# Kernel tuning notes

Measured on AMD Instinct MI355X. Metric: run time of the kernel, lower is better.

The kernel has to match this reference:

```python
import jax, jax.numpy as jnp
import numpy as np

B, H, S, DK = 2, 8, 4096, 64


def setup_inputs() -> dict:
    key = jax.random.key(0)
    kq, kk, kv = jax.random.split(key, 3)
    Q = jax.random.normal(kq, (B, H, S, DK), dtype=jnp.float32)
    K = jax.random.normal(kk, (B, H, S, DK), dtype=jnp.float32)
    V = jax.random.normal(kv, (B, H, S, DK), dtype=jnp.float32)
    attn_mask = jnp.zeros((1,), dtype=bool)  # accepted but unused by the module
    return {"Q": Q, "K": K, "V": V, "attn_mask": attn_mask}


def reference(Q, K, V, attn_mask):
    d_k = Q.shape[-1]
    scale = 1.0 / np.sqrt(d_k).astype(np.float32)
    # scores: [b, h, q, k] -- full O(n^2) matrix, as in the original
    scores = jnp.einsum('bhqd,bhkd->bhqk', Q, K) * scale
    attn = jax.nn.softmax(scores, axis=-1)
    context = jnp.einsum('bhqk,bhkd->bhqd', attn, V)
    return (context, attn)
```

## Files before the change

### kernel.cpp

```cpp
#include <hip/hip_runtime.h>
#include <hip/hip_bf16.h>


typedef __bf16 bf16x8 __attribute__((ext_vector_type(8)));
typedef __bf16 bf16x4 __attribute__((ext_vector_type(4)));
typedef float f32x4 __attribute__((ext_vector_type(4)));

#define BH 16
#define SEQ 4096
#define DKD 64
#define PSTRIDE 72
#define LOG2E 1.44269504088896f

__global__ void cvt_bf16_kernel(const float* __restrict__ src,
                                __bf16* __restrict__ dst, int n4, float scale) {
    int i = blockIdx.x * blockDim.x + threadIdx.x;
    if (i < n4) {
        const float4 v = reinterpret_cast<const float4*>(src)[i];
        bf16x4 o;
        o[0] = (__bf16)(v.x * scale); o[1] = (__bf16)(v.y * scale);
        o[2] = (__bf16)(v.z * scale); o[3] = (__bf16)(v.w * scale);
        reinterpret_cast<bf16x4*>(dst)[i] = o;
    }
}

__global__ void transpose_v_kernel(const float* __restrict__ V,
                                   __bf16* __restrict__ Vt) {
    __shared__ __bf16 T[DKD][72];
    const int head = blockIdx.y;
    const int s0 = blockIdx.x * 64;
    const int t = threadIdx.x;
    const float* vp = V + ((size_t)head * SEQ + s0) * DKD;
#pragma unroll
    for (int i = 0; i < 16; ++i) {
        int j = i * 256 + t;
        T[j & 63][j >> 6] = (__bf16)vp[j];
    }
    __syncthreads();
    __bf16* op = Vt + (size_t)head * DKD * SEQ + s0;
#pragma unroll
    for (int i = 0; i < 16; ++i) {
        int j = i * 256 + t;
        op[(size_t)(j >> 6) * SEQ + (j & 63)] = T[j >> 6][j & 63];
    }
}

__global__ __launch_bounds__(256, 4) void attn_kernel(
    const __bf16* __restrict__ Qb, const __bf16* __restrict__ Kb,
    const __bf16* __restrict__ Vt, float* __restrict__ out_ctx,
    float* __restrict__ out_attn) {
    __shared__ __align__(16) __bf16 Pl[2][4][16][PSTRIDE];

    const int tid = threadIdx.x;
    const int w = tid >> 6;
    const int lane = tid & 63;
    const int c16 = lane & 15;
    const int g = lane >> 4;

    const int wg = blockIdx.x;
    const int head = ((wg & 7) << 1) | ((wg >> 3) & 1);
    const int qt = wg >> 4;
    const int qbase = qt * 64 + w * 16;

    const __bf16* qp = Qb + ((size_t)head * SEQ + qbase + c16) * DKD + g * 8;
    const bf16x8 qf0 = *reinterpret_cast<const bf16x8*>(qp);
    const bf16x8 qf1 = *reinterpret_cast<const bf16x8*>(qp + 32);

    const __bf16* kbase = Kb + (size_t)head * SEQ * DKD;
    const __bf16* vbase = Vt + (size_t)head * DKD * SEQ;
    float* attn_p = out_attn + ((size_t)head * SEQ + qbase) * SEQ;

    float lsum = 0.f;
    auto loadK = [&](bf16x8 (&kf)[8], int tile) {
        const int kt = tile * 64;
#pragma unroll
        for (int ct = 0; ct < 4; ++ct) {
            const __bf16* kp = kbase + (size_t)(kt + ct * 16 + c16) * DKD + g * 8;
            kf[ct * 2] = *reinterpret_cast<const bf16x8*>(kp);
            kf[ct * 2 + 1] = *reinterpret_cast<const bf16x8*>(kp + 32);
        }
    };
    auto procA = [&](const bf16x8 (&kf)[8]) {
#pragma unroll
        for (int ct = 0; ct < 4; ++ct) {
            f32x4 a = (f32x4){0.f, 0.f, 0.f, 0.f};
            a = __builtin_amdgcn_mfma_f32_16x16x32_bf16(kf[ct * 2], qf0, a, 0, 0, 0);
            a = __builtin_amdgcn_mfma_f32_16x16x32_bf16(kf[ct * 2 + 1], qf1, a, 0, 0, 0);
            float e0 = __builtin_amdgcn_exp2f(a[0] * LOG2E);
            float e1 = __builtin_amdgcn_exp2f(a[1] * LOG2E);
            float e2 = __builtin_amdgcn_exp2f(a[2] * LOG2E);
            float e3 = __builtin_amdgcn_exp2f(a[3] * LOG2E);
            lsum += (e0 + e1) + (e2 + e3);
        }
    };
    {
        bf16x8 kA[8], kB[8];
        loadK(kA, 0);
        for (int t = 0; t < 64; t += 2) {
            loadK(kB, t + 1);
            procA(kA);
            loadK(kA, (t + 2) & 63);
            procA(kB);
        }
    }
    lsum += __shfl_xor(lsum, 16);
    lsum += __shfl_xor(lsum, 32);
    const float inv_l = __builtin_amdgcn_rcpf(lsum);

    f32x4 o[4];
#pragma unroll
    for (int dt = 0; dt < 4; ++dt) o[dt] = (f32x4){0.f, 0.f, 0.f, 0.f};

    auto computeS = [&](int tile, __bf16(*Pbuf)[PSTRIDE]) {
        const int kt = tile * 64;
        f32x4 acc[4];
#pragma unroll
        for (int ct = 0; ct < 4; ++ct) {
            acc[ct] = (f32x4){0.f, 0.f, 0.f, 0.f};
            const __bf16* kp = kbase + (size_t)(kt + ct * 16 + c16) * DKD + g * 8;
            bf16x8 kf0 = *reinterpret_cast<const bf16x8*>(kp);
            bf16x8 kf1 = *reinterpret_cast<const bf16x8*>(kp + 32);
            acc[ct] = __builtin_amdgcn_mfma_f32_16x16x32_bf16(kf0, qf0, acc[ct], 0, 0, 0);
            acc[ct] = __builtin_amdgcn_mfma_f32_16x16x32_bf16(kf1, qf1, acc[ct], 0, 0, 0);
        }
#pragma unroll
        for (int ct = 0; ct < 4; ++ct) {
            bf16x4 pb;
#pragma unroll
            for (int r = 0; r < 4; ++r)
                pb[r] = (__bf16)(__builtin_amdgcn_exp2f(acc[ct][r] * LOG2E) * inv_l);
            *reinterpret_cast<bf16x4*>(&Pbuf[c16][ct * 16 + g * 4]) = pb;
        }
    };

    auto storeAttn = [&](int tile, const __bf16(*Pbuf)[PSTRIDE]) {
        const int kt = tile * 64;
#pragma unroll
        for (int r4 = 0; r4 < 4; ++r4) {
            const int row = r4 * 4 + g;
            bf16x4 pb = *reinterpret_cast<const bf16x4*>(&Pbuf[row][c16 * 4]);
            f32x4 v;
#pragma unroll
            for (int j = 0; j < 4; ++j) v[j] = (float)pb[j];
            __builtin_nontemporal_store(
                v, reinterpret_cast<f32x4*>(attn_p + (size_t)row * SEQ + kt + c16 * 4));
        }
    };

    auto pvTile = [&](int tile, const __bf16(*Pbuf)[PSTRIDE]) {
        const int kt = tile * 64;
        bf16x8 pb0 = *reinterpret_cast<const bf16x8*>(&Pbuf[c16][g * 8]);
        bf16x8 pb1 = *reinterpret_cast<const bf16x8*>(&Pbuf[c16][g * 8 + 32]);
#pragma unroll
        for (int dt = 0; dt < 4; ++dt) {
            const __bf16* vp = vbase + (size_t)(dt * 16 + c16) * SEQ + kt + g * 8;
            bf16x8 vf0 = *reinterpret_cast<const bf16x8*>(vp);
            bf16x8 vf1 = *reinterpret_cast<const bf16x8*>(vp + 32);
            o[dt] = __builtin_amdgcn_mfma_f32_16x16x32_bf16(vf0, pb0, o[dt], 0, 0, 0);
            o[dt] = __builtin_amdgcn_mfma_f32_16x16x32_bf16(vf1, pb1, o[dt], 0, 0, 0);
        }
    };

    computeS(0, Pl[0][w]);
    for (int t = 1; t < 63; t += 2) {
        computeS(t, Pl[1][w]);
        storeAttn(t - 1, Pl[0][w]);
        pvTile(t - 1, Pl[0][w]);
        computeS(t + 1, Pl[0][w]);
        storeAttn(t, Pl[1][w]);
        pvTile(t, Pl[1][w]);
    }
    computeS(63, Pl[1][w]);
    storeAttn(62, Pl[0][w]);
    pvTile(62, Pl[0][w]);
    storeAttn(63, Pl[1][w]);
    pvTile(63, Pl[1][w]);

    float* ctx_p = out_ctx + ((size_t)head * SEQ + qbase) * DKD;
#pragma unroll
    for (int dt = 0; dt < 4; ++dt)
        *reinterpret_cast<f32x4*>(ctx_p + (size_t)c16 * DKD + dt * 16 + g * 4) = o[dt];
}

extern "C" void kernel_launch(void* const* d_in, const int* in_sizes, int n_in,
                              void* d_out, int out_size, void* d_ws, size_t ws_size,
                              hipStream_t stream) {
    const float* Q = (const float*)d_in[0];
    const float* K = (const float*)d_in[1];
    const float* V = (const float*)d_in[2];
    float* out = (float*)d_out;

    const size_t nElem = (size_t)BH * SEQ * DKD;
    __bf16* Qb = (__bf16*)d_ws;
    __bf16* Kb = Qb + nElem;
    __bf16* Vt = Kb + nElem;

    float* out_ctx = out;
    float* out_attn = out + nElem;

    const int n4 = (int)(nElem / 4);
    cvt_bf16_kernel<<<dim3((n4 + 255) / 256), dim3(256), 0, stream>>>(Q, Qb, n4, 0.125f);
    cvt_bf16_kernel<<<dim3((n4 + 255) / 256), dim3(256), 0, stream>>>(K, Kb, n4, 1.0f);
    transpose_v_kernel<<<dim3(64, BH), dim3(256), 0, stream>>>(V, Vt);
    attn_kernel<<<dim3(BH * SEQ / 64), dim3(256), 0, stream>>>(Qb, Kb, Vt, out_ctx, out_attn);
}
```

Measured before the change: 728.6 us.

## Split key range across wave pairs with cross-wave reduction of row sums and context

Each block now covers 32 query rows instead of 64. Two waves share each 16-row slice and each handles half of the key tiles. Row-sum partials are combined through shared memory after a barrier, and the partial context accumulators are reduced through LDS before the final write. The grid doubles and launch bounds are raised to 8 blocks per unit. The hand-pipelined K prefetch in the first pass is dropped, and attention stores become regular stores instead of nontemporal ones. Together these aim for more parallelism and occupancy, at the cost of extra barriers, LDS traffic and possible register pressure.

```diff
diff --git a/kernel.cpp b/kernel.cpp
--- a/kernel.cpp
+++ b/kernel.cpp
@@ -45,22 +45,26 @@
     }
 }
 
-__global__ __launch_bounds__(256, 4) void attn_kernel(
+__global__ __launch_bounds__(256, 8) void attn_kernel(
     const __bf16* __restrict__ Qb, const __bf16* __restrict__ Kb,
     const __bf16* __restrict__ Vt, float* __restrict__ out_ctx,
     float* __restrict__ out_attn) {
     __shared__ __align__(16) __bf16 Pl[2][4][16][PSTRIDE];
+    __shared__ float Lsum[4][16];
 
     const int tid = threadIdx.x;
     const int w = tid >> 6;
     const int lane = tid & 63;
     const int c16 = lane & 15;
     const int g = lane >> 4;
+    const int qsub = w & 1;
+    const int khalf = w >> 1;
 
     const int wg = blockIdx.x;
     const int head = ((wg & 7) << 1) | ((wg >> 3) & 1);
-    const int qt = wg >> 4;
-    const int qbase = qt * 64 + w * 16;
+    const int qblk = wg >> 4;
+    const int qbase = qblk * 32 + qsub * 16;
+    const int tile0 = khalf * 32;
 
     const __bf16* qp = Qb + ((size_t)head * SEQ + qbase + c16) * DKD + g * 8;
     const bf16x8 qf0 = *reinterpret_cast<const bf16x8*>(qp);
@@ -71,48 +75,35 @@
     float* attn_p = out_attn + ((size_t)head * SEQ + qbase) * SEQ;
 
     float lsum = 0.f;
-    auto loadK = [&](bf16x8 (&kf)[8], int tile) {
-        const int kt = tile * 64;
+    for (int t = 0; t < 32; ++t) {
+        const int kt = (tile0 + t) * 64;
 #pragma unroll
         for (int ct = 0; ct < 4; ++ct) {
             const __bf16* kp = kbase + (size_t)(kt + ct * 16 + c16) * DKD + g * 8;
-            kf[ct * 2] = *reinterpret_cast<const bf16x8*>(kp);
-            kf[ct * 2 + 1] = *reinterpret_cast<const bf16x8*>(kp + 32);
-        }
-    };
-    auto procA = [&](const bf16x8 (&kf)[8]) {
-#pragma unroll
-        for (int ct = 0; ct < 4; ++ct) {
+            bf16x8 kf0 = *reinterpret_cast<const bf16x8*>(kp);
+            bf16x8 kf1 = *reinterpret_cast<const bf16x8*>(kp + 32);
             f32x4 a = (f32x4){0.f, 0.f, 0.f, 0.f};
-            a = __builtin_amdgcn_mfma_f32_16x16x32_bf16(kf[ct * 2], qf0, a, 0, 0, 0);
-            a = __builtin_amdgcn_mfma_f32_16x16x32_bf16(kf[ct * 2 + 1], qf1, a, 0, 0, 0);
+            a = __builtin_amdgcn_mfma_f32_16x16x32_bf16(kf0, qf0, a, 0, 0, 0);
+            a = __builtin_amdgcn_mfma_f32_16x16x32_bf16(kf1, qf1, a, 0, 0, 0);
             float e0 = __builtin_amdgcn_exp2f(a[0] * LOG2E);
             float e1 = __builtin_amdgcn_exp2f(a[1] * LOG2E);
             float e2 = __builtin_amdgcn_exp2f(a[2] * LOG2E);
             float e3 = __builtin_amdgcn_exp2f(a[3] * LOG2E);
             lsum += (e0 + e1) + (e2 + e3);
         }
-    };
-    {
-        bf16x8 kA[8], kB[8];
-        loadK(kA, 0);
-        for (int t = 0; t < 64; t += 2) {
-            loadK(kB, t + 1);
-            procA(kA);
-            loadK(kA, (t + 2) & 63);
-            procA(kB);
-        }
     }
     lsum += __shfl_xor(lsum, 16);
     lsum += __shfl_xor(lsum, 32);
-    const float inv_l = __builtin_amdgcn_rcpf(lsum);
+    if (g == 0) Lsum[w][c16] = lsum;
+    __syncthreads();
+    const float inv_l = __builtin_amdgcn_rcpf(Lsum[w][c16] + Lsum[w ^ 2][c16]);
 
     f32x4 o[4];
 #pragma unroll
     for (int dt = 0; dt < 4; ++dt) o[dt] = (f32x4){0.f, 0.f, 0.f, 0.f};
 
-    auto computeS = [&](int tile, __bf16(*Pbuf)[PSTRIDE]) {
-        const int kt = tile * 64;
+    auto computeS = [&](int t, __bf16(*Pbuf)[PSTRIDE]) {
+        const int kt = (tile0 + t) * 64;
         f32x4 acc[4];
 #pragma unroll
         for (int ct = 0; ct < 4; ++ct) {
@@ -133,22 +124,8 @@
         }
     };
 
-    auto storeAttn = [&](int tile, const __bf16(*Pbuf)[PSTRIDE]) {
-        const int kt = tile * 64;
-#pragma unroll
-        for (int r4 = 0; r4 < 4; ++r4) {
-            const int row = r4 * 4 + g;
-            bf16x4 pb = *reinterpret_cast<const bf16x4*>(&Pbuf[row][c16 * 4]);
-            f32x4 v;
-#pragma unroll
-            for (int j = 0; j < 4; ++j) v[j] = (float)pb[j];
-            __builtin_nontemporal_store(
-                v, reinterpret_cast<f32x4*>(attn_p + (size_t)row * SEQ + kt + c16 * 4));
-        }
-    };
-
-    auto pvTile = [&](int tile, const __bf16(*Pbuf)[PSTRIDE]) {
-        const int kt = tile * 64;
+    auto pvTile = [&](int t, const __bf16(*Pbuf)[PSTRIDE]) {
+        const int kt = (tile0 + t) * 64;
         bf16x8 pb0 = *reinterpret_cast<const bf16x8*>(&Pbuf[c16][g * 8]);
         bf16x8 pb1 = *reinterpret_cast<const bf16x8*>(&Pbuf[c16][g * 8 + 32]);
 #pragma unroll
@@ -161,25 +138,52 @@
         }
     };
 
+    auto storeAttn = [&](int t, const __bf16(*Pbuf)[PSTRIDE]) {
+        const int kt = (tile0 + t) * 64;
+#pragma unroll
+        for (int r4 = 0; r4 < 4; ++r4) {
+            const int row = r4 * 4 + g;
+            bf16x4 pb = *reinterpret_cast<const bf16x4*>(&Pbuf[row][c16 * 4]);
+            f32x4 v;
+#pragma unroll
+            for (int j = 0; j < 4; ++j) v[j] = (float)pb[j];
+            *reinterpret_cast<f32x4*>(attn_p + (size_t)row * SEQ + kt + c16 * 4) = v;
+        }
+    };
+
     computeS(0, Pl[0][w]);
-    for (int t = 1; t < 63; t += 2) {
+    for (int t = 1; t < 31; t += 2) {
         computeS(t, Pl[1][w]);
+        pvTile(t - 1, Pl[0][w]);
         storeAttn(t - 1, Pl[0][w]);
-        pvTile(t - 1, Pl[0][w]);
         computeS(t + 1, Pl[0][w]);
+        pvTile(t, Pl[1][w]);
         storeAttn(t, Pl[1][w]);
-        pvTile(t, Pl[1][w]);
-    }
-    computeS(63, Pl[1][w]);
-    storeAttn(62, Pl[0][w]);
-    pvTile(62, Pl[0][w]);
-    storeAttn(63, Pl[1][w]);
-    pvTile(63, Pl[1][w]);
-
-    float* ctx_p = out_ctx + ((size_t)head * SEQ + qbase) * DKD;
-#pragma unroll
-    for (int dt = 0; dt < 4; ++dt)
-        *reinterpret_cast<f32x4*>(ctx_p + (size_t)c16 * DKD + dt * 16 + g * 4) = o[dt];
+    }
+    computeS(31, Pl[1][w]);
+    pvTile(30, Pl[0][w]);
+    storeAttn(30, Pl[0][w]);
+    pvTile(31, Pl[1][w]);
+    storeAttn(31, Pl[1][w]);
+
+    __syncthreads();
+    float* Of = reinterpret_cast<float*>(&Pl[0][0][0][0]);
+    float* my = Of + ((size_t)qsub * 16 + c16) * 64;
+    if (khalf == 1) {
+#pragma unroll
+        for (int dt = 0; dt < 4; ++dt)
+            *reinterpret_cast<f32x4*>(my + dt * 16 + g * 4) = o[dt];
+    }
+    __syncthreads();
+    if (khalf == 0) {
+        float* ctx_p = out_ctx + ((size_t)head * SEQ + qbase) * DKD;
+#pragma unroll
+        for (int dt = 0; dt < 4; ++dt) {
+            f32x4 p = *reinterpret_cast<const f32x4*>(my + dt * 16 + g * 4);
+            o[dt] += p;
+            *reinterpret_cast<f32x4*>(ctx_p + (size_t)c16 * DKD + dt * 16 + g * 4) = o[dt];
+        }
+    }
 }
 
 extern "C" void kernel_launch(void* const* d_in, const int* in_sizes, int n_in,
@@ -202,5 +206,5 @@
     cvt_bf16_kernel<<<dim3((n4 + 255) / 256), dim3(256), 0, stream>>>(Q, Qb, n4, 0.125f);
     cvt_bf16_kernel<<<dim3((n4 + 255) / 256), dim3(256), 0, stream>>>(K, Kb, n4, 1.0f);
     transpose_v_kernel<<<dim3(64, BH), dim3(256), 0, stream>>>(V, Vt);
-    attn_kernel<<<dim3(BH * SEQ / 64), dim3(256), 0, stream>>>(Qb, Kb, Vt, out_ctx, out_attn);
-}
+    attn_kernel<<<dim3(BH * SEQ / 32), dim3(256), 0, stream>>>(Qb, Kb, Vt, out_ctx, out_attn);
+}
```

Result: slower. 964.1 us (+32.3%).
